# Performance work log

Measured on AMD Instinct MI355X. Metric: run time of the kernel, lower is better.

Reference implementation:

```python
import jax, jax.numpy as jnp
import numpy as np

N_TOKENS = 32768
DIM = 2048
N_EXPERTS = 64
TOP_K = 8
N_GROUP = 8
TOPK_GROUP = 4
ROUTE_SCALE = 2.5
EPS = 1e-20


def setup_inputs() -> dict:
    key = jax.random.key(0)
    k1, k2 = jax.random.split(key)
    hidden_states = jax.random.normal(k1, (N_TOKENS, DIM), dtype=jnp.float32)
    weight = jax.random.normal(k2, (N_EXPERTS, DIM), dtype=jnp.float32) * 0.02
    e_score_correction_bias = jnp.zeros((N_EXPERTS,), dtype=jnp.float32)
    return {"hidden_states": hidden_states, "weight": weight,
            "e_score_correction_bias": e_score_correction_bias}


def reference(hidden_states, weight, e_score_correction_bias):
    # router logits in fp32: [N, E]
    logits = jnp.einsum('nd,ed->ne', hidden_states.astype(jnp.float32),
                        weight.astype(jnp.float32))
    scores = jax.nn.sigmoid(logits)  # score_func == 'sigmoid'

    # --- top-k index selection (no-grad path in torch) ---
    sfc = scores + e_score_correction_bias[None, :]  # [N, E]
    per_group = N_EXPERTS // N_GROUP
    # group score = sum of top-2 scores within each group: [N, G]
    grouped = sfc.reshape(-1, N_GROUP, per_group)
    group_scores = jax.lax.top_k(grouped, 2)[0].sum(axis=-1)
    # pick top `TOPK_GROUP` groups
    _, group_idx = jax.lax.top_k(group_scores, TOPK_GROUP)  # [N, topk_group]
    n = group_scores.shape[0]
    group_mask = jnp.zeros_like(group_scores).at[
        jnp.arange(n)[:, None], group_idx].set(1.0)  # [N, G]
    score_mask = jnp.repeat(group_mask, per_group, axis=1)  # [N, E]
    masked_scores = jnp.where(score_mask > 0, sfc, 0.0)
    _, topk_indices = jax.lax.top_k(masked_scores, TOP_K)  # [N, top_k]

    # gather weights from *unbiased* scores, normalize, scale
    topk_weights = jnp.take_along_axis(scores, topk_indices, axis=1)
    denom = topk_weights.sum(axis=-1, keepdims=True) + EPS
    topk_weights = topk_weights / denom * ROUTE_SCALE
    return topk_indices, topk_weights
```

## Files before the change

### kernel.cpp

```cpp
#include <hip/hip_runtime.h>
#include <math.h>

#define NT 32768
#define DIM 2048
#define NE 64
#define RSCALE 2.5f
#define REPS 1e-20f
#define KC 32
#define NCH (DIM / KC)
#define TOK 64

typedef const __attribute__((address_space(1))) void GV;
typedef __attribute__((address_space(3))) void LV;
typedef __attribute__((ext_vector_type(8))) short short8x;
typedef __attribute__((ext_vector_type(4))) float f32x4;
typedef __attribute__((ext_vector_type(4))) unsigned int uint4x;
typedef __attribute__((ext_vector_type(2))) unsigned int uint2x;

#define HS_FLOATS 2048
#define WL_OFF 16384
#define WL_PITCH 40
#define WL_LIMB (64 * WL_PITCH)
#define WL_BUF (3 * WL_LIMB)
#define BS_OFF 47104
#define ARENA_BYTES 47424

#define PACKHI(odd, even) __builtin_amdgcn_perm((odd), (even), 0x07060302u)

__device__ __forceinline__ void decomp4(f32x4 x, unsigned int o[6]) {
    unsigned int u0 = __float_as_uint(x.x), u1 = __float_as_uint(x.y);
    unsigned int u2 = __float_as_uint(x.z), u3 = __float_as_uint(x.w);
    o[0] = PACKHI(u1, u0); o[1] = PACKHI(u3, u2);
    float r0 = x.x - __uint_as_float(u0 & 0xffff0000u);
    float r1 = x.y - __uint_as_float(u1 & 0xffff0000u);
    float r2 = x.z - __uint_as_float(u2 & 0xffff0000u);
    float r3 = x.w - __uint_as_float(u3 & 0xffff0000u);
    unsigned int v0 = __float_as_uint(r0), v1 = __float_as_uint(r1);
    unsigned int v2 = __float_as_uint(r2), v3 = __float_as_uint(r3);
    o[2] = PACKHI(v1, v0); o[3] = PACKHI(v3, v2);
    float s0 = r0 - __uint_as_float(v0 & 0xffff0000u);
    float s1 = r1 - __uint_as_float(v1 & 0xffff0000u);
    float s2 = r2 - __uint_as_float(v2 & 0xffff0000u);
    float s3 = r3 - __uint_as_float(v3 & 0xffff0000u);
    o[4] = PACKHI(__float_as_uint(s1), __float_as_uint(s0));
    o[5] = PACKHI(__float_as_uint(s3), __float_as_uint(s2));
}

__device__ __forceinline__ void decomp8(f32x4 a, f32x4 b,
                                        short8x* f0, short8x* f1, short8x* f2) {
    unsigned int oa[6], ob[6];
    decomp4(a, oa); decomp4(b, ob);
    uint4x t0 = {oa[0], oa[1], ob[0], ob[1]};
    uint4x t1 = {oa[2], oa[3], ob[2], ob[3]};
    uint4x t2 = {oa[4], oa[5], ob[4], ob[5]};
    *f0 = __builtin_bit_cast(short8x, t0);
    *f1 = __builtin_bit_cast(short8x, t1);
    *f2 = __builtin_bit_cast(short8x, t2);
}

__global__ __launch_bounds__(256) void router_kernel(
    const float* __restrict__ H,
    const float* __restrict__ W,
    const float* __restrict__ B,
    float* __restrict__ out)
{
    __shared__ __align__(16) char arena[ARENA_BYTES];
    float* hsf = (float*)(arena);
    short* wl  = (short*)(arena + WL_OFF);
    float* bsf = (float*)(arena + BS_OFF);
    float* scf = (float*)(arena);

    const int tid  = threadIdx.x;
    const int lane = tid & 63;
    const int w    = tid >> 6;
    const size_t tb = (size_t)blockIdx.x * TOK;

    if (tid < NE) bsf[tid] = B[tid];

    const int l15 = lane & 15, g = lane >> 4, l7 = lane & 7;
    const int tg = (w & 1) * 32, eg = (w >> 1) * 32;

    const int sp = lane & 7, ro = lane >> 3;
    const float* hg0 = H + (tb + (size_t)(w * 16 + ro)) * DIM + ((sp ^ ro) << 2);
    const float* hg1 = H + (tb + (size_t)(w * 16 + 8 + ro)) * DIM + ((sp ^ ro) << 2);
    const int hb0 = (w * 16) * KC * 4;
    const int hb1 = (w * 16 + 8) * KC * 4;

    const int we0 = tid >> 3, wq0 = tid & 7;

    f32x4 Cm[2][2], Cc[2][2];
    double md[2][2][4];
    #pragma unroll
    for (int a = 0; a < 2; ++a)
        #pragma unroll
        for (int b = 0; b < 2; ++b) {
            Cm[a][b] = (f32x4)0.0f; Cc[a][b] = (f32x4)0.0f;
            #pragma unroll
            for (int r = 0; r < 4; ++r) md[a][b][r] = 0.0;
        }

    {
        __builtin_amdgcn_global_load_lds((GV*)hg0, (LV*)(arena + hb0), 16, 0, 0);
        __builtin_amdgcn_global_load_lds((GV*)hg1, (LV*)(arena + hb1), 16, 0, 0);
        f32x4 wv0 = *(const f32x4*)&W[(size_t)we0 * DIM + wq0 * 4];
        f32x4 wv1 = *(const f32x4*)&W[(size_t)(we0 + 32) * DIM + wq0 * 4];
        unsigned int o[6];
        decomp4(wv0, o);
        #pragma unroll
        for (int L = 0; L < 3; ++L)
            *(uint2x*)&wl[L * WL_LIMB + we0 * WL_PITCH + wq0 * 4] =
                (uint2x){o[2 * L], o[2 * L + 1]};
        decomp4(wv1, o);
        #pragma unroll
        for (int L = 0; L < 3; ++L)
            *(uint2x*)&wl[L * WL_LIMB + (we0 + 32) * WL_PITCH + wq0 * 4] =
                (uint2x){o[2 * L], o[2 * L + 1]};
    }
    __syncthreads();

    for (int ch = 0; ch < NCH; ++ch) {
        const int p = ch & 1;
        const bool pre = (ch + 1) < NCH;

        f32x4 wv0, wv1;
        if (pre) {
            const int kn = (ch + 1) * KC;
            __builtin_amdgcn_global_load_lds((GV*)(hg0 + kn),
                (LV*)(arena + (p ^ 1) * HS_FLOATS * 4 + hb0), 16, 0, 0);
            __builtin_amdgcn_global_load_lds((GV*)(hg1 + kn),
                (LV*)(arena + (p ^ 1) * HS_FLOATS * 4 + hb1), 16, 0, 0);
            wv0 = *(const f32x4*)&W[(size_t)we0 * DIM + kn + wq0 * 4];
            wv1 = *(const f32x4*)&W[(size_t)(we0 + 32) * DIM + kn + wq0 * 4];
        }

        short8x af[2][3];
        #pragma unroll
        for (int tt = 0; tt < 2; ++tt) {
            const int t = tg + tt * 16 + l15;
            const float* hr = &hsf[p * HS_FLOATS + t * KC];
            f32x4 xa = *(const f32x4*)&hr[((g * 2) ^ l7) << 2];
            f32x4 xb = *(const f32x4*)&hr[((g * 2 + 1) ^ l7) << 2];
            decomp8(xa, xb, &af[tt][0], &af[tt][1], &af[tt][2]);
        }

        const short* wlp = &wl[p * WL_BUF];
        #pragma unroll
        for (int et = 0; et < 2; ++et) {
            const int e = eg + et * 16 + l15;
            short8x b0 = *(const short8x*)&wlp[0 * WL_LIMB + e * WL_PITCH + g * 8];
            short8x b1 = *(const short8x*)&wlp[1 * WL_LIMB + e * WL_PITCH + g * 8];
            short8x b2 = *(const short8x*)&wlp[2 * WL_LIMB + e * WL_PITCH + g * 8];
            #pragma unroll
            for (int tt = 0; tt < 2; ++tt) {
                Cm[tt][et] = __builtin_amdgcn_mfma_f32_16x16x32_bf16(af[tt][0], b0, Cm[tt][et], 0, 0, 0);
                Cc[tt][et] = __builtin_amdgcn_mfma_f32_16x16x32_bf16(af[tt][1], b0, Cc[tt][et], 0, 0, 0);
                Cc[tt][et] = __builtin_amdgcn_mfma_f32_16x16x32_bf16(af[tt][2], b0, Cc[tt][et], 0, 0, 0);
                Cc[tt][et] = __builtin_amdgcn_mfma_f32_16x16x32_bf16(af[tt][0], b1, Cc[tt][et], 0, 0, 0);
                Cc[tt][et] = __builtin_amdgcn_mfma_f32_16x16x32_bf16(af[tt][1], b1, Cc[tt][et], 0, 0, 0);
                Cc[tt][et] = __builtin_amdgcn_mfma_f32_16x16x32_bf16(af[tt][0], b2, Cc[tt][et], 0, 0, 0);
            }
        }

        if (pre) {
            short* wn = &wl[(p ^ 1) * WL_BUF];
            unsigned int o[6];
            decomp4(wv0, o);
            #pragma unroll
            for (int L = 0; L < 3; ++L)
                *(uint2x*)&wn[L * WL_LIMB + we0 * WL_PITCH + wq0 * 4] =
                    (uint2x){o[2 * L], o[2 * L + 1]};
            decomp4(wv1, o);
            #pragma unroll
            for (int L = 0; L < 3; ++L)
                *(uint2x*)&wn[L * WL_LIMB + (we0 + 32) * WL_PITCH + wq0 * 4] =
                    (uint2x){o[2 * L], o[2 * L + 1]};
        }

        if ((ch & 7) == 7) {
            #pragma unroll
            for (int tt = 0; tt < 2; ++tt)
                #pragma unroll
                for (int et = 0; et < 2; ++et) {
                    #pragma unroll
                    for (int r = 0; r < 4; ++r)
                        md[tt][et][r] += (double)Cm[tt][et][r] + (double)Cc[tt][et][r];
                    Cm[tt][et] = (f32x4)0.0f;
                    Cc[tt][et] = (f32x4)0.0f;
                }
        }
        __syncthreads();
    }

    #pragma unroll
    for (int tt = 0; tt < 2; ++tt)
        #pragma unroll
        for (int et = 0; et < 2; ++et)
            #pragma unroll
            for (int r = 0; r < 4; ++r) {
                float logit = (float)md[tt][et][r];
                float s = 1.0f / (1.0f + expf(-logit));
                int t = tg + tt * 16 + g * 4 + r;
                int e = eg + et * 16 + l15;
                scf[t * 65 + e] = s;
            }
    __syncthreads();

    if ((tid & 3) == 0) {
        const int t = tid >> 2;
        const float* sc = &scf[t * 65];
        float gs[8];
        #pragma unroll
        for (int gg = 0; gg < 8; ++gg) {
            float m1 = -1e30f, m2 = -1e30f;
            #pragma unroll
            for (int j = 0; j < 8; ++j) {
                float v = sc[gg * 8 + j] + bsf[gg * 8 + j];
                if (v > m1) { m2 = m1; m1 = v; }
                else if (v > m2) { m2 = v; }
            }
            gs[gg] = m1 + m2;
        }
        unsigned gmask = 0;
        for (int i = 0; i < 4; ++i) {
            float best = -1e30f; int bg = 0;
            for (int gg = 0; gg < 8; ++gg)
                if (!((gmask >> gg) & 1u) && gs[gg] > best) { best = gs[gg]; bg = gg; }
            gmask |= 1u << bg;
        }
        unsigned long long picked = 0ull;
        int   idxs[8];
        float wts[8];
        float wsum = 0.0f;
        for (int i = 0; i < 8; ++i) {
            float best = -1e30f; int bi = 0;
            for (int e = 0; e < 64; ++e) {
                if ((picked >> e) & 1ull) continue;
                float v = ((gmask >> (e >> 3)) & 1u) ? (sc[e] + bsf[e]) : 0.0f;
                if (v > best) { best = v; bi = e; }
            }
            picked |= 1ull << bi;
            idxs[i] = bi;
            wts[i] = sc[bi];
            wsum += sc[bi];
        }
        const float scale = RSCALE / (wsum + REPS);
        const size_t token = tb + t;
        #pragma unroll
        for (int i = 0; i < 8; ++i) {
            out[token * 8 + i] = (float)idxs[i];
            out[(size_t)NT * 8 + token * 8 + i] = wts[i] * scale;
        }
    }
}

extern "C" void kernel_launch(void* const* d_in, const int* in_sizes, int n_in,
                              void* d_out, int out_size, void* d_ws, size_t ws_size,
                              hipStream_t stream) {
    (void)in_sizes; (void)n_in; (void)out_size; (void)d_ws; (void)ws_size;
    const float* H = (const float*)d_in[0];
    const float* W = (const float*)d_in[1];
    const float* B = (const float*)d_in[2];
    float* out = (float*)d_out;
    router_kernel<<<dim3(NT / TOK), dim3(256), 0, stream>>>(H, W, B, out);
}
```

Baseline: 137.7 us.

## Predecompose hidden states into bf16 limbs in LDS with 512-thread specialized staging

Doubles the block to 512 threads. The first half loads and splits hidden-state rows into three bf16 limbs and the second half does the same for weights, both written into swizzled LDS buffers. This replaces per-wave redundant decomposition of the activation tile and the global_load_lds path. Each wave now computes one 16-token by 32-expert tile, with a register-held two-stage prefetch pipeline that unrolls the chunk loop by two. The cost is more LDS per block, higher register pressure from the staging registers, and a fixed 4-blocks-per-CU launch bound.

```diff
diff --git a/kernel.cpp b/kernel.cpp
--- a/kernel.cpp
+++ b/kernel.cpp
@@ -10,20 +10,14 @@
 #define NCH (DIM / KC)
 #define TOK 64
 
-typedef const __attribute__((address_space(1))) void GV;
-typedef __attribute__((address_space(3))) void LV;
+#define HL_BUF 12288
+#define WL_OFF 24576
+#define BS_OFF 49152
+#define ARENA 49408
+
 typedef __attribute__((ext_vector_type(8))) short short8x;
 typedef __attribute__((ext_vector_type(4))) float f32x4;
 typedef __attribute__((ext_vector_type(4))) unsigned int uint4x;
-typedef __attribute__((ext_vector_type(2))) unsigned int uint2x;
-
-#define HS_FLOATS 2048
-#define WL_OFF 16384
-#define WL_PITCH 40
-#define WL_LIMB (64 * WL_PITCH)
-#define WL_BUF (3 * WL_LIMB)
-#define BS_OFF 47104
-#define ARENA_BYTES 47424
 
 #define PACKHI(odd, even) __builtin_amdgcn_perm((odd), (even), 0x07060302u)
 
@@ -58,155 +52,126 @@
     *f2 = __builtin_bit_cast(short8x, t2);
 }
 
-__global__ __launch_bounds__(256) void router_kernel(
+#define STAGE_ISSUE(SA, SB, KOFF) do { \
+    SA = *(const f32x4*)(gsrc + (KOFF));     \
+    SB = *(const f32x4*)(gsrc + (KOFF) + 4); \
+} while (0)
+
+#define STAGE_WRITE(SA, SB, PN) do { \
+    short8x f0_, f1_, f2_; \
+    decomp8(SA, SB, &f0_, &f1_, &f2_); \
+    *(short8x*)(arena + sbase + (PN) * HL_BUF + 0 * 4096 + soff) = f0_; \
+    *(short8x*)(arena + sbase + (PN) * HL_BUF + 1 * 4096 + soff) = f1_; \
+    *(short8x*)(arena + sbase + (PN) * HL_BUF + 2 * 4096 + soff) = f2_; \
+} while (0)
+
+#define COMPUTE(P) do { \
+    const char* hb = arena + (P) * HL_BUF; \
+    const char* wb = arena + WL_OFF + (P) * HL_BUF; \
+    short8x a0, a1, a2; \
+    { const int t_ = tt * 16 + l15; \
+      const int ro_ = t_ * 64 + ((g ^ ((t_ >> 1) & 3)) << 4); \
+      a0 = *(const short8x*)(hb + 0 * 4096 + ro_); \
+      a1 = *(const short8x*)(hb + 1 * 4096 + ro_); \
+      a2 = *(const short8x*)(hb + 2 * 4096 + ro_); } \
+    _Pragma("unroll") \
+    for (int et = 0; et < 2; ++et) { \
+        const int e_ = ep * 32 + et * 16 + l15; \
+        const int ro_ = e_ * 64 + ((g ^ ((e_ >> 1) & 3)) << 4); \
+        short8x b0 = *(const short8x*)(wb + 0 * 4096 + ro_); \
+        short8x b1 = *(const short8x*)(wb + 1 * 4096 + ro_); \
+        short8x b2 = *(const short8x*)(wb + 2 * 4096 + ro_); \
+        Cm[et] = __builtin_amdgcn_mfma_f32_16x16x32_bf16(a0, b0, Cm[et], 0, 0, 0); \
+        Cc[et] = __builtin_amdgcn_mfma_f32_16x16x32_bf16(a1, b0, Cc[et], 0, 0, 0); \
+        Cc[et] = __builtin_amdgcn_mfma_f32_16x16x32_bf16(a2, b0, Cc[et], 0, 0, 0); \
+        Cc[et] = __builtin_amdgcn_mfma_f32_16x16x32_bf16(a0, b1, Cc[et], 0, 0, 0); \
+        Cc[et] = __builtin_amdgcn_mfma_f32_16x16x32_bf16(a1, b1, Cc[et], 0, 0, 0); \
+        Cc[et] = __builtin_amdgcn_mfma_f32_16x16x32_bf16(a0, b2, Cc[et], 0, 0, 0); \
+    } \
+} while (0)
+
+#define DRAIN do { \
+    _Pragma("unroll") \
+    for (int et = 0; et < 2; ++et) { \
+        _Pragma("unroll") \
+        for (int r = 0; r < 4; ++r) \
+            md[et][r] += (double)Cm[et][r] + (double)Cc[et][r]; \
+        Cm[et] = (f32x4)0.0f; Cc[et] = (f32x4)0.0f; \
+    } \
+} while (0)
+
+__global__ __launch_bounds__(512, 4) void router_kernel(
     const float* __restrict__ H,
     const float* __restrict__ W,
     const float* __restrict__ B,
     float* __restrict__ out)
 {
-    __shared__ __align__(16) char arena[ARENA_BYTES];
-    float* hsf = (float*)(arena);
-    short* wl  = (short*)(arena + WL_OFF);
+    __shared__ __align__(16) char arena[ARENA];
     float* bsf = (float*)(arena + BS_OFF);
     float* scf = (float*)(arena);
 
     const int tid  = threadIdx.x;
     const int lane = tid & 63;
-    const int w    = tid >> 6;
+    const int w    = __builtin_amdgcn_readfirstlane(tid >> 6);
+    const int l15  = lane & 15, g = lane >> 4;
     const size_t tb = (size_t)blockIdx.x * TOK;
 
     if (tid < NE) bsf[tid] = B[tid];
 
-    const int l15 = lane & 15, g = lane >> 4, l7 = lane & 7;
-    const int tg = (w & 1) * 32, eg = (w >> 1) * 32;
-
-    const int sp = lane & 7, ro = lane >> 3;
-    const float* hg0 = H + (tb + (size_t)(w * 16 + ro)) * DIM + ((sp ^ ro) << 2);
-    const float* hg1 = H + (tb + (size_t)(w * 16 + 8 + ro)) * DIM + ((sp ^ ro) << 2);
-    const int hb0 = (w * 16) * KC * 4;
-    const int hb1 = (w * 16 + 8) * KC * 4;
-
-    const int we0 = tid >> 3, wq0 = tid & 7;
-
-    f32x4 Cm[2][2], Cc[2][2];
-    double md[2][2][4];
+    const int si   = tid & 255;
+    const int srow = si >> 2;
+    const int sq   = si & 3;
+    const bool isH = tid < 256;
+    const float* gsrc = isH ? (H + (tb + (size_t)srow) * DIM + sq * 8)
+                            : (W + (size_t)srow * DIM + sq * 8);
+    const int sbase = isH ? 0 : WL_OFF;
+    const int soff  = srow * 64 + ((sq ^ ((srow >> 1) & 3)) << 4);
+
+    const int tt = w & 3, ep = w >> 2;
+
+    f32x4 Cm[2], Cc[2];
+    double md[2][4];
     #pragma unroll
-    for (int a = 0; a < 2; ++a)
-        #pragma unroll
-        for (int b = 0; b < 2; ++b) {
-            Cm[a][b] = (f32x4)0.0f; Cc[a][b] = (f32x4)0.0f;
-            #pragma unroll
-            for (int r = 0; r < 4; ++r) md[a][b][r] = 0.0;
-        }
-
-    {
-        __builtin_amdgcn_global_load_lds((GV*)hg0, (LV*)(arena + hb0), 16, 0, 0);
-        __builtin_amdgcn_global_load_lds((GV*)hg1, (LV*)(arena + hb1), 16, 0, 0);
-        f32x4 wv0 = *(const f32x4*)&W[(size_t)we0 * DIM + wq0 * 4];
-        f32x4 wv1 = *(const f32x4*)&W[(size_t)(we0 + 32) * DIM + wq0 * 4];
-        unsigned int o[6];
-        decomp4(wv0, o);
-        #pragma unroll
-        for (int L = 0; L < 3; ++L)
-            *(uint2x*)&wl[L * WL_LIMB + we0 * WL_PITCH + wq0 * 4] =
-                (uint2x){o[2 * L], o[2 * L + 1]};
-        decomp4(wv1, o);
-        #pragma unroll
-        for (int L = 0; L < 3; ++L)
-            *(uint2x*)&wl[L * WL_LIMB + (we0 + 32) * WL_PITCH + wq0 * 4] =
-                (uint2x){o[2 * L], o[2 * L + 1]};
+    for (int et = 0; et < 2; ++et) {
+        Cm[et] = (f32x4)0.0f; Cc[et] = (f32x4)0.0f;
+        #pragma unroll
+        for (int r = 0; r < 4; ++r) md[et][r] = 0.0;
     }
+
+    f32x4 sA0, sA1, sB0, sB1;
+
+    STAGE_ISSUE(sA0, sA1, 0);
+    STAGE_WRITE(sA0, sA1, 0);
+    STAGE_ISSUE(sB0, sB1, KC);
     __syncthreads();
 
-    for (int ch = 0; ch < NCH; ++ch) {
-        const int p = ch & 1;
-        const bool pre = (ch + 1) < NCH;
-
-        f32x4 wv0, wv1;
-        if (pre) {
-            const int kn = (ch + 1) * KC;
-            __builtin_amdgcn_global_load_lds((GV*)(hg0 + kn),
-                (LV*)(arena + (p ^ 1) * HS_FLOATS * 4 + hb0), 16, 0, 0);
-            __builtin_amdgcn_global_load_lds((GV*)(hg1 + kn),
-                (LV*)(arena + (p ^ 1) * HS_FLOATS * 4 + hb1), 16, 0, 0);
-            wv0 = *(const f32x4*)&W[(size_t)we0 * DIM + kn + wq0 * 4];
-            wv1 = *(const f32x4*)&W[(size_t)(we0 + 32) * DIM + kn + wq0 * 4];
-        }
-
-        short8x af[2][3];
-        #pragma unroll
-        for (int tt = 0; tt < 2; ++tt) {
-            const int t = tg + tt * 16 + l15;
-            const float* hr = &hsf[p * HS_FLOATS + t * KC];
-            f32x4 xa = *(const f32x4*)&hr[((g * 2) ^ l7) << 2];
-            f32x4 xb = *(const f32x4*)&hr[((g * 2 + 1) ^ l7) << 2];
-            decomp8(xa, xb, &af[tt][0], &af[tt][1], &af[tt][2]);
-        }
-
-        const short* wlp = &wl[p * WL_BUF];
-        #pragma unroll
-        for (int et = 0; et < 2; ++et) {
-            const int e = eg + et * 16 + l15;
-            short8x b0 = *(const short8x*)&wlp[0 * WL_LIMB + e * WL_PITCH + g * 8];
-            short8x b1 = *(const short8x*)&wlp[1 * WL_LIMB + e * WL_PITCH + g * 8];
-            short8x b2 = *(const short8x*)&wlp[2 * WL_LIMB + e * WL_PITCH + g * 8];
-            #pragma unroll
-            for (int tt = 0; tt < 2; ++tt) {
-                Cm[tt][et] = __builtin_amdgcn_mfma_f32_16x16x32_bf16(af[tt][0], b0, Cm[tt][et], 0, 0, 0);
-                Cc[tt][et] = __builtin_amdgcn_mfma_f32_16x16x32_bf16(af[tt][1], b0, Cc[tt][et], 0, 0, 0);
-                Cc[tt][et] = __builtin_amdgcn_mfma_f32_16x16x32_bf16(af[tt][2], b0, Cc[tt][et], 0, 0, 0);
-                Cc[tt][et] = __builtin_amdgcn_mfma_f32_16x16x32_bf16(af[tt][0], b1, Cc[tt][et], 0, 0, 0);
-                Cc[tt][et] = __builtin_amdgcn_mfma_f32_16x16x32_bf16(af[tt][1], b1, Cc[tt][et], 0, 0, 0);
-                Cc[tt][et] = __builtin_amdgcn_mfma_f32_16x16x32_bf16(af[tt][0], b2, Cc[tt][et], 0, 0, 0);
-            }
-        }
-
-        if (pre) {
-            short* wn = &wl[(p ^ 1) * WL_BUF];
-            unsigned int o[6];
-            decomp4(wv0, o);
-            #pragma unroll
-            for (int L = 0; L < 3; ++L)
-                *(uint2x*)&wn[L * WL_LIMB + we0 * WL_PITCH + wq0 * 4] =
-                    (uint2x){o[2 * L], o[2 * L + 1]};
-            decomp4(wv1, o);
-            #pragma unroll
-            for (int L = 0; L < 3; ++L)
-                *(uint2x*)&wn[L * WL_LIMB + (we0 + 32) * WL_PITCH + wq0 * 4] =
-                    (uint2x){o[2 * L], o[2 * L + 1]};
-        }
-
-        if ((ch & 7) == 7) {
-            #pragma unroll
-            for (int tt = 0; tt < 2; ++tt)
-                #pragma unroll
-                for (int et = 0; et < 2; ++et) {
-                    #pragma unroll
-                    for (int r = 0; r < 4; ++r)
-                        md[tt][et][r] += (double)Cm[tt][et][r] + (double)Cc[tt][et][r];
-                    Cm[tt][et] = (f32x4)0.0f;
-                    Cc[tt][et] = (f32x4)0.0f;
-                }
-        }
+    for (int chb = 0; chb < NCH; chb += 2) {
+        if (chb + 2 < NCH) STAGE_ISSUE(sA0, sA1, (chb + 2) * KC);
+        COMPUTE(0);
+        STAGE_WRITE(sB0, sB1, 1);
+        __syncthreads();
+
+        if (chb + 3 < NCH) STAGE_ISSUE(sB0, sB1, (chb + 3) * KC);
+        COMPUTE(1);
+        if (chb + 2 < NCH) STAGE_WRITE(sA0, sA1, 0);
+        if (((chb + 1) & 7) == 7) DRAIN;
         __syncthreads();
     }
 
     #pragma unroll
-    for (int tt = 0; tt < 2; ++tt)
-        #pragma unroll
-        for (int et = 0; et < 2; ++et)
-            #pragma unroll
-            for (int r = 0; r < 4; ++r) {
-                float logit = (float)md[tt][et][r];
-                float s = 1.0f / (1.0f + expf(-logit));
-                int t = tg + tt * 16 + g * 4 + r;
-                int e = eg + et * 16 + l15;
-                scf[t * 65 + e] = s;
-            }
+    for (int et = 0; et < 2; ++et)
+        #pragma unroll
+        for (int r = 0; r < 4; ++r) {
+            float logit = (float)md[et][r];
+            float s = 1.0f / (1.0f + expf(-logit));
+            int t = tt * 16 + g * 4 + r;
+            int e = ep * 32 + et * 16 + l15;
+            scf[t * 65 + e] = s;
+        }
     __syncthreads();
 
-    if ((tid & 3) == 0) {
-        const int t = tid >> 2;
+    if ((tid & 7) == 0) {
+        const int t = tid >> 3;
         const float* sc = &scf[t * 65];
         float gs[8];
         #pragma unroll
@@ -261,5 +226,5 @@
     const float* W = (const float*)d_in[1];
     const float* B = (const float*)d_in[2];
     float* out = (float*)d_out;
-    router_kernel<<<dim3(NT / TOK), dim3(256), 0, stream>>>(H, W, B, out);
-}
+    router_kernel<<<dim3(NT / TOK), dim3(512), 0, stream>>>(H, W, B, out);
+}
```

After: 142.0 us. 3.1% more time.
